# Kernel tuning notes

Hardware: AMD Instinct MI355X
Metric: run time of the kernel (lower is better)

Reference implementation:

```python
import jax, jax.numpy as jnp
import numpy as np
import math

D = 128      # out_dim (= d)
H = 4        # n_heads
DK = D // H  # d_k = 32
M = 5        # fixed num types in forward
NN = 15      # fixed N in forward
SQRT_DK = math.sqrt(DK)


def setup_inputs() -> dict:
    key = jax.random.key(0)
    ks = jax.random.split(key, 18)
    b, n = 1024, 64
    inp = {
        "node_inp": jax.random.normal(ks[0], (D, b, n), jnp.float32),
        "WW": jax.random.normal(ks[1], (b, M, n, NN), jnp.float32) * 0.1,
        "mask_matrix": jax.random.uniform(ks[2], (M * NN, n), jnp.float32),
        "R": jax.random.normal(ks[3], (b, H, n, n), jnp.float32),
        "attn_mask": jax.random.uniform(ks[4], (1, 1, n, 4 * n), jnp.float32),
        # learned parameters (xavier-ish scale)
        "WK": jax.random.normal(ks[5], (M, D, D), jnp.float32) * 0.05,
        "bK": jax.random.normal(ks[6], (M, D, 1), jnp.float32) * 0.05,
        "WQ": jax.random.normal(ks[7], (M, D, D), jnp.float32) * 0.05,
        "bQ": jax.random.normal(ks[8], (M, D, 1), jnp.float32) * 0.05,
        "WM": jax.random.normal(ks[9], (M, D, D), jnp.float32) * 0.05,
        "bM": jax.random.normal(ks[10], (M, D, 1), jnp.float32) * 0.05,
        "WB": jax.random.normal(ks[11], (M, D, D), jnp.float32) * 0.05,
        "bB": jax.random.normal(ks[12], (M, D, 1), jnp.float32) * 0.05,
        "Wmsgup": jax.random.normal(ks[13], (DK, DK), jnp.float32) * 0.1,
        "Wmsgdown": jax.random.normal(ks[14], (DK, DK), jnp.float32) * 0.1,
        "Wmsgleft": jax.random.normal(ks[15], (DK, DK), jnp.float32) * 0.1,
        "Wmsgright": jax.random.normal(ks[16], (DK, DK), jnp.float32) * 0.1,
    }
    return inp


def reference(node_inp, WW, mask_matrix, R, attn_mask,
              WK, bK, WQ, bQ, WM, bM, WB, bB,
              Wmsgup, Wmsgdown, Wmsgleft, Wmsgright):
    d, b, n = node_inp.shape
    # project node features through per-type mixing: (b, m, d, N)
    node_inp_m = jnp.einsum('dbn,bmnN->bmdN', node_inp, WW)

    def proj_perm(W, bias):
        # per-type linear then permute(0,2,1,3) before flatten (as K/Q do)
        x = jnp.einsum('mde,bmeN->bmdN', W, node_inp_m) + bias[None]  # (b,m,d,N)
        x = x.transpose(0, 2, 1, 3).reshape(b, d, M * NN)
        return x @ mask_matrix  # (b, d, n)

    K = proj_perm(WK, bK).reshape(b, H, DK, n)
    Q = proj_perm(WQ, bQ).reshape(b, H, DK, n)

    # message: NOTE original reshapes (b*m,d,N) -> (b,d,m*N) WITHOUT the permute; replicate faithfully
    msg = jnp.einsum('mde,bmeN->bmdN', WM, node_inp_m) + bM[None]  # (b,m,d,N)
    message = msg.reshape(b, d, M * NN) @ mask_matrix               # (b, d, n)

    A = jnp.einsum('bhki,bhkj->bhij', Q, K) / SQRT_DK               # (b,h,n,n)
    aw = jax.nn.softmax(R + A, axis=3)
    aw = jnp.where(jnp.isnan(aw), jnp.zeros_like(aw), aw)
    aw = jnp.tile(aw, (1, 1, 1, 4)) * attn_mask                     # (b,h,n,4n)

    res_msg = message.reshape(b, H, DK, n)
    Wmsg = jnp.concatenate([Wmsgup, Wmsgdown, Wmsgleft, Wmsgright], axis=1)  # (dk, 4dk)
    res = jnp.einsum('kq,bhkn->bhqn', Wmsg, res_msg)                # (b,h,4dk,n)
    res = res.reshape(b, H, DK, 4 * n)                               # faithful reshape

    B = jnp.einsum('bhnm,bhkm->bhkn', aw, res).reshape(b, d, n)
    B = jax.nn.gelu(B, approximate=False)

    Bm = jnp.einsum('bdn,bmnN->bmdN', B, WW)
    Bm = jnp.einsum('mde,bmeN->bmdN', WB, Bm) + bB[None]
    Bm = Bm.transpose(0, 2, 1, 3).reshape(b, d, M * NN) @ mask_matrix  # (b,d,n)
    out = Bm.transpose(1, 0, 2) + node_inp                             # (d,b,n)
    return (out, aw[0, 0])
```

## Files before the change

kernel.cpp:

```cpp
#include <hip/hip_runtime.h>
#include <math.h>

#define Dd 128
#define Hh 4
#define DKk 32
#define Mm 5
#define NNn 15
#define Bb 1024
#define Nn 64
#define MN 75
#define BN 65536
#define RSQRT_DK 0.17677669529663687f

typedef __attribute__((ext_vector_type(8))) short bf16x8;
typedef __attribute__((ext_vector_type(4))) float f32x4;

__device__ __forceinline__ ushort f2bf(float x) {
    unsigned u = __float_as_uint(x);
    u = (u + 0x7fffu + ((u >> 16) & 1u)) >> 16;
    return (ushort)u;
}
__device__ __forceinline__ float bf2f(ushort h) {
    return __uint_as_float(((unsigned)h) << 16);
}
__device__ __forceinline__ void split2(float x, ushort& hi, ushort& lo) {
    hi = f2bf(x);
    lo = f2bf(x - bf2f(hi));
}
__device__ __forceinline__ f32x4 MFMA(bf16x8 a, bf16x8 b, f32x4 c) {
    return __builtin_amdgcn_mfma_f32_16x16x32_bf16(a, b, c, 0, 0, 0);
}

__global__ void k0_prep(const float* __restrict__ maskm,
                        const float* __restrict__ WK, const float* __restrict__ bK,
                        const float* __restrict__ WQ, const float* __restrict__ bQ,
                        const float* __restrict__ WM, const float* __restrict__ bM,
                        const float* __restrict__ WB, const float* __restrict__ bB,
                        const float* __restrict__ Wu, const float* __restrict__ Wd,
                        const float* __restrict__ Wl, const float* __restrict__ Wr,
                        ushort* __restrict__ WKhi, ushort* __restrict__ WKlo,
                        ushort* __restrict__ WQhi, ushort* __restrict__ WQlo,
                        ushort* __restrict__ WMhi, ushort* __restrict__ WBhi,
                        ushort* __restrict__ maskhi, ushort* __restrict__ masklo,
                        ushort* __restrict__ maskThi, ushort* __restrict__ maskTlo,
                        float* __restrict__ btKT, float* __restrict__ btQT,
                        float* __restrict__ btMT, float* __restrict__ btB,
                        ushort* __restrict__ WcatT)
{
    int tid = blockIdx.x * blockDim.x + threadIdx.x;
    int nthr = gridDim.x * blockDim.x;
    const int NW = Mm * Dd * Dd;
    for (int i = tid; i < NW; i += nthr) {
        split2(WK[i], WKhi[i], WKlo[i]);
        split2(WQ[i], WQhi[i], WQlo[i]);
        WMhi[i] = f2bf(WM[i]);
        WBhi[i] = f2bf(WB[i]);
    }
    for (int i = tid; i < 96 * 64; i += nthr) {
        float v = (i < MN * 64) ? maskm[i] : 0.f;
        split2(v, maskhi[i], masklo[i]);
    }
    for (int i = tid; i < 64 * 96; i += nthr) {
        int col = i / 96, j = i - col * 96;
        float v = (j < MN) ? maskm[j * 64 + col] : 0.f;
        split2(v, maskThi[i], maskTlo[i]);
    }
    for (int i = tid; i < 4096; i += nthr) {
        int q = i >> 5, kk = i & 31;
        const float* Wsel = (q < 32) ? Wu : (q < 64) ? Wd : (q < 96) ? Wl : Wr;
        WcatT[i] = f2bf(Wsel[kk * 32 + (q & 31)]);
    }
    for (int i = tid; i < 8192; i += nthr) {
        int d = i >> 6, col = i & 63;
        float aKv = 0.f, aQv = 0.f, aBv = 0.f;
        for (int m = 0; m < Mm; ++m) {
            float mrs = 0.f;
            for (int N = 0; N < NNn; ++N) mrs += maskm[(m * 15 + N) * 64 + col];
            aKv += bK[m * 128 + d] * mrs;
            aQv += bQ[m * 128 + d] * mrs;
            aBv += bB[m * 128 + d] * mrs;
        }
        btKT[col * 128 + d] = aKv;
        btQT[col * 128 + d] = aQv;
        btB[i] = aBv;
        float aMv = 0.f;
        for (int j = 0; j < MN; ++j) {
            int f = d * 75 + j;
            int m = f / 1920;
            int dloc = (f / 15) & 127;
            aMv += bM[m * 128 + dloc] * maskm[j * 64 + col];
        }
        btMT[col * 128 + d] = aMv;
    }
}

__global__ __launch_bounds__(512, 4) void k1_proj(
    const float* __restrict__ node, const float* __restrict__ WW,
    const ushort* __restrict__ WKhi, const ushort* __restrict__ WKlo,
    const ushort* __restrict__ WQhi, const ushort* __restrict__ WQlo,
    const ushort* __restrict__ WMhi,
    const ushort* __restrict__ maskThi, const ushort* __restrict__ maskTlo,
    const float* __restrict__ btKT, const float* __restrict__ btQT,
    const float* __restrict__ btMT,
    ushort* __restrict__ Khi, ushort* __restrict__ Klo,
    ushort* __restrict__ Qhi, ushort* __restrict__ Qlo,
    ushort* __restrict__ msgTg)
{
    const int b = blockIdx.x;
    const int tid = threadIdx.x;
    const int lane = tid & 63, w = tid >> 6;
    const int l15 = lane & 15, lq = lane >> 4;

    __shared__ ushort nimTh[80 * 136];
    __shared__ ushort nimTl[80 * 136];
    __shared__ ushort planes[4 * 32 * 104];

    ushort* Ykh = planes;
    ushort* Ykl = planes + 32 * 104;
    ushort* Yqh = planes + 2 * 32 * 104;
    ushort* Yql = planes + 3 * 32 * 104;

    for (int t = tid; t < 5 * 136; t += 512) {
        int mm = t / 136, e = t - mm * 136;
        nimTh[(mm * 16 + 15) * 136 + e] = 0;
        nimTl[(mm * 16 + 15) * 136 + e] = 0;
    }
    for (int t = tid; t < 128 * 29; t += 512) {
        int r = t / 29, cc = 75 + (t - r * 29);
        planes[r * 104 + cc] = 0;
    }

    const f32x4 zz = {0.f, 0.f, 0.f, 0.f};

    {
        bf16x8 ah[2], al[2];
        #pragma unroll
        for (int ks = 0; ks < 2; ++ks) {
            const float* np = node + (size_t)(w * 16 + l15) * BN + b * 64 + ks * 32 + lq * 8;
            float tmp[8];
            *(float4*)tmp       = *(const float4*)np;
            *(float4*)(tmp + 4) = *(const float4*)(np + 4);
            #pragma unroll
            for (int j = 0; j < 8; ++j) {
                ushort h_, l_; split2(tmp[j], h_, l_);
                ah[ks][j] = (short)h_; al[ks][j] = (short)l_;
            }
        }
        for (int m = 0; m < Mm; ++m) {
            const float* wp = WW + ((size_t)b * Mm + m) * 960 + (l15 < 15 ? l15 : 0);
            f32x4 chh = zz, chl = zz, clh = zz;
            #pragma unroll
            for (int ks = 0; ks < 2; ++ks) {
                bf16x8 bh, bl;
                #pragma unroll
                for (int t = 0; t < 8; ++t) {
                    int n = ks * 32 + lq * 8 + t;
                    float v = (l15 < 15) ? wp[n * 15] : 0.f;
                    ushort h_, l_; split2(v, h_, l_);
                    bh[t] = (short)h_; bl[t] = (short)l_;
                }
                chh = MFMA(ah[ks], bh, chh);
                chl = MFMA(ah[ks], bl, chl);
                clh = MFMA(al[ks], bh, clh);
            }
            f32x4 c = chh + chl + clh;
            if (l15 < 15) {
                #pragma unroll
                for (int t = 0; t < 4; ++t) {
                    int e = w * 16 + lq * 4 + t;
                    split2(c[t], nimTh[(m * 16 + l15) * 136 + e],
                                 nimTl[(m * 16 + l15) * 136 + e]);
                }
            }
        }
    }
    __syncthreads();

    for (int qd = 0; qd < 4; ++qd) {
        for (int u = w; u < 10; u += 8) {
            int m = u >> 1, rt = u & 1;
            int d0 = qd * 32 + rt * 16 + l15;
            f32x4 khh = zz, khl = zz, klh = zz;
            f32x4 qhh = zz, qhl = zz, qlh = zz;
            #pragma unroll
            for (int ks = 0; ks < 4; ++ks) {
                int k0 = ks * 32 + lq * 8;
                size_t wo = (size_t)m * 16384 + (size_t)d0 * 128 + k0;
                bf16x8 akh = *(const bf16x8*)(WKhi + wo);
                bf16x8 akl = *(const bf16x8*)(WKlo + wo);
                bf16x8 aqh = *(const bf16x8*)(WQhi + wo);
                bf16x8 aql = *(const bf16x8*)(WQlo + wo);
                bf16x8 bh = *(const bf16x8*)(&nimTh[(m * 16 + l15) * 136 + k0]);
                bf16x8 bl = *(const bf16x8*)(&nimTl[(m * 16 + l15) * 136 + k0]);
                khh = MFMA(akh, bh, khh); khl = MFMA(akh, bl, khl); klh = MFMA(akl, bh, klh);
                qhh = MFMA(aqh, bh, qhh); qhl = MFMA(aqh, bl, qhl); qlh = MFMA(aql, bh, qlh);
            }
            f32x4 cK = khh + khl + klh;
            f32x4 cQ = qhh + qhl + qlh;
            if (l15 < 15) {
                int j = m * 15 + l15;
                #pragma unroll
                for (int t = 0; t < 4; ++t) {
                    int r = rt * 16 + lq * 4 + t;
                    split2(cK[t], Ykh[r * 104 + j], Ykl[r * 104 + j]);
                    split2(cQ[t], Yqh[r * 104 + j], Yql[r * 104 + j]);
                }
            }
        }
        __syncthreads();
        {
            int nr = w & 3, dc = w >> 2;
            f32x4 khh = zz, khl = zz, klh = zz;
            f32x4 qhh = zz, qhl = zz, qlh = zz;
            #pragma unroll
            for (int ks = 0; ks < 3; ++ks) {
                int k0 = ks * 32 + lq * 8;
                bf16x8 mh = *(const bf16x8*)(maskThi + (nr * 16 + l15) * 96 + k0);
                bf16x8 ml = *(const bf16x8*)(maskTlo + (nr * 16 + l15) * 96 + k0);
                bf16x8 ykh = *(const bf16x8*)(&Ykh[(dc * 16 + l15) * 104 + k0]);
                bf16x8 ykl = *(const bf16x8*)(&Ykl[(dc * 16 + l15) * 104 + k0]);
                bf16x8 yqh = *(const bf16x8*)(&Yqh[(dc * 16 + l15) * 104 + k0]);
                bf16x8 yql = *(const bf16x8*)(&Yql[(dc * 16 + l15) * 104 + k0]);
                khh = MFMA(mh, ykh, khh); khl = MFMA(ml, ykh, khl); klh = MFMA(mh, ykl, klh);
                qhh = MFMA(mh, yqh, qhh); qhl = MFMA(ml, yqh, qhl); qlh = MFMA(mh, yql, qlh);
            }
            f32x4 cK = khh + khl + klh;
            f32x4 cQ = qhh + qhl + qlh;
            #pragma unroll
            for (int t = 0; t < 4; ++t) {
                int n = nr * 16 + lq * 4 + t;
                int dloc = dc * 16 + l15;
                int d = qd * 32 + dloc;
                size_t oi = (((size_t)(b * 4 + qd)) * 64 + n) * 32 + dloc;
                ushort hh_, ll_;
                split2(cK[t] + btKT[n * 128 + d], hh_, ll_);
                Khi[oi] = hh_; Klo[oi] = ll_;
                split2(cQ[t] + btQT[n * 128 + d], hh_, ll_);
                Qhi[oi] = hh_; Qlo[oi] = ll_;
            }
        }
        __syncthreads();
    }

    {
        int rt = w;
        for (int m = 0; m < Mm; ++m) {
            f32x4 c0 = zz, c1 = zz;
            #pragma unroll
            for (int ks = 0; ks < 4; ++ks) {
                int k0 = ks * 32 + lq * 8;
                bf16x8 a  = *(const bf16x8*)(WMhi + (size_t)m * 16384 + (size_t)(rt * 16 + l15) * 128 + k0);
                bf16x8 bh = *(const bf16x8*)(&nimTh[(m * 16 + l15) * 136 + k0]);
                if (ks < 2) c0 = MFMA(a, bh, c0); else c1 = MFMA(a, bh, c1);
            }
            f32x4 c = c0 + c1;
            if (l15 < 15) {
                #pragma unroll
                for (int t = 0; t < 4; ++t) {
                    int dflat = rt * 16 + lq * 4 + t;
                    int g = m * 1920 + dflat * 15 + l15;
                    planes[(g / 75) * 104 + (g % 75)] = f2bf(c[t]);
                }
            }
        }
    }
    __syncthreads();
    #pragma unroll
    for (int s = 0; s < 4; ++s) {
        int u = w * 4 + s;
        int nr = u & 3, ddc = u >> 2;
        f32x4 cs0 = zz, cs1 = zz, cs2 = zz;
        {
            bf16x8 a0 = *(const bf16x8*)(maskThi + (nr * 16 + l15) * 96 + lq * 8);
            bf16x8 b0 = *(const bf16x8*)(&planes[(ddc * 16 + l15) * 104 + lq * 8]);
            cs0 = MFMA(a0, b0, cs0);
            bf16x8 a1 = *(const bf16x8*)(maskThi + (nr * 16 + l15) * 96 + 32 + lq * 8);
            bf16x8 b1 = *(const bf16x8*)(&planes[(ddc * 16 + l15) * 104 + 32 + lq * 8]);
            cs1 = MFMA(a1, b1, cs1);
            bf16x8 a2 = *(const bf16x8*)(maskThi + (nr * 16 + l15) * 96 + 64 + lq * 8);
            bf16x8 b2 = *(const bf16x8*)(&planes[(ddc * 16 + l15) * 104 + 64 + lq * 8]);
            cs2 = MFMA(a2, b2, cs2);
        }
        f32x4 c = cs0 + cs1 + cs2;
        #pragma unroll
        for (int t = 0; t < 4; ++t) {
            int n = nr * 16 + lq * 4 + t;
            int dd = ddc * 16 + l15;
            int h = dd >> 5, dk = dd & 31;
            msgTg[(((size_t)(b * 4 + h)) * 64 + n) * 32 + dk] = f2bf(c[t] + btMT[n * 128 + dd]);
        }
    }
}

__global__ __launch_bounds__(512, 4) void k2_attn(
    const ushort* __restrict__ Khi, const ushort* __restrict__ Klo,
    const ushort* Qhi, const ushort* __restrict__ Qlo,
    const ushort* __restrict__ msgTg,
    const float* __restrict__ R, const float* __restrict__ am,
    const ushort* __restrict__ WcatT, float* __restrict__ aw00,
    ushort* Bout)
{
    const int b = blockIdx.x >> 2, h = blockIdx.x & 3;
    const int tid = threadIdx.x;
    const int lane = tid & 63, w = tid >> 6;
    const int l15 = lane & 15, lq = lane >> 4;

    __shared__ float  ST[64 * 65];
    __shared__ ushort resS[128 * 72];
    __shared__ ushort awq[64 * 72];

    const f32x4 zz = {0.f, 0.f, 0.f, 0.f};
    const size_t base2 = (size_t)(b * 4 + h) * 2048;
    const float* Rb = R + (size_t)(b * 4 + h) * 4096;

    {
        int ti = w >> 1;
        bf16x8 ah = *(const bf16x8*)(Qhi + base2 + (size_t)(ti * 16 + l15) * 32 + lq * 8);
        bf16x8 al = *(const bf16x8*)(Qlo + base2 + (size_t)(ti * 16 + l15) * 32 + lq * 8);
        #pragma unroll
        for (int s = 0; s < 2; ++s) {
            int tj = (w & 1) * 2 + s;
            bf16x8 bh = *(const bf16x8*)(Khi + base2 + (size_t)(tj * 16 + l15) * 32 + lq * 8);
            bf16x8 bl = *(const bf16x8*)(Klo + base2 + (size_t)(tj * 16 + l15) * 32 + lq * 8);
            f32x4 chh = zz, chl = zz, clh = zz;
            chh = MFMA(ah, bh, chh); chl = MFMA(ah, bl, chl); clh = MFMA(al, bh, clh);
            f32x4 c = chh + chl + clh;
            #pragma unroll
            for (int r = 0; r < 4; ++r) {
                int i = ti * 16 + lq * 4 + r, j = tj * 16 + l15;
                ST[j * 65 + i] = Rb[i * 64 + j] + c[r] * RSQRT_DK;
            }
        }
    }
    {
        bf16x8 a = *(const bf16x8*)(WcatT + (w * 16 + l15) * 32 + lq * 8);
        #pragma unroll
        for (int nt = 0; nt < 4; ++nt) {
            bf16x8 bfr = *(const bf16x8*)(msgTg + base2 + (size_t)(nt * 16 + l15) * 32 + lq * 8);
            f32x4 c = MFMA(a, bfr, zz);
            #pragma unroll
            for (int r = 0; r < 4; ++r)
                resS[(w * 16 + lq * 4 + r) * 72 + nt * 16 + l15] = f2bf(c[r]);
        }
    }
    __syncthreads();

    {
        int row = tid >> 3, part = tid & 7;
        float v[8]; float mx = -INFINITY;
        #pragma unroll
        for (int jj = 0; jj < 8; ++jj) { v[jj] = ST[(part * 8 + jj) * 65 + row]; mx = fmaxf(mx, v[jj]); }
        mx = fmaxf(mx, __shfl_xor(mx, 1));
        mx = fmaxf(mx, __shfl_xor(mx, 2));
        mx = fmaxf(mx, __shfl_xor(mx, 4));
        float s = 0.f;
        #pragma unroll
        for (int jj = 0; jj < 8; ++jj) { v[jj] = expf(v[jj] - mx); s += v[jj]; }
        s += __shfl_xor(s, 1); s += __shfl_xor(s, 2); s += __shfl_xor(s, 4);
        float inv = 1.f / s;
        #pragma unroll
        for (int jj = 0; jj < 8; ++jj) {
            float p = v[jj] * inv;
            ST[(part * 8 + jj) * 65 + row] = isnan(p) ? 0.f : p;
        }
    }
    __syncthreads();

    const int kt = w >> 2, it = w & 3;
    f32x4 accB0 = zz, accB1 = zz;
    for (int q = 0; q < 4; ++q) {
        for (int e = tid; e < 4096; e += 512) {
            int i = e >> 6, j0 = e & 63;
            float p = ST[j0 * 65 + i] * am[i * 256 + q * 64 + j0];
            awq[i * 72 + j0] = f2bf(p);
            if (blockIdx.x == 0) aw00[i * 256 + q * 64 + j0] = p;
        }
        __syncthreads();
        int row = 4 * (kt * 16 + l15) + q;
        bf16x8 a0 = *(const bf16x8*)(&resS[row * 72 + lq * 8]);
        bf16x8 b0 = *(const bf16x8*)(&awq[(it * 16 + l15) * 72 + lq * 8]);
        accB0 = MFMA(a0, b0, accB0);
        bf16x8 a1 = *(const bf16x8*)(&resS[row * 72 + 32 + lq * 8]);
        bf16x8 b1 = *(const bf16x8*)(&awq[(it * 16 + l15) * 72 + 32 + lq * 8]);
        accB1 = MFMA(a1, b1, accB1);
        __syncthreads();
    }
    f32x4 accB = accB0 + accB1;

    #pragma unroll
    for (int r = 0; r < 4; ++r) {
        int k = kt * 16 + lq * 4 + r, i = it * 16 + l15;
        float x = accB[r];
        float g = 0.5f * x * (1.f + erff(x * 0.70710678118654752f));
        Bout[base2 + k * 64 + i] = f2bf(g);
    }
}

__global__ __launch_bounds__(512, 4) void k3_out(
    const ushort* Bbuf, const float* __restrict__ WW,
    const ushort* __restrict__ WBhi, const ushort* __restrict__ maskhi,
    const float* __restrict__ btB, const float* __restrict__ node,
    float* __restrict__ outp)
{
    const int b = blockIdx.x, tid = threadIdx.x;
    const int lane = tid & 63, w = tid >> 6, l15 = lane & 15, lq = lane >> 4;
    __shared__ ushort sB[128 * 72];
    __shared__ ushort wwh[64 * 17];
    __shared__ ushort t1[128 * 17];
    __shared__ ushort nm[32 * 66];

    for (int i = tid; i < 8192; i += 512) {
        int d = i >> 6, n = i & 63;
        sB[d * 72 + n] = Bbuf[(size_t)b * 8192 + i];
    }
    const f32x4 zz = {0.f, 0.f, 0.f, 0.f};
    f32x4 acc[4];
    for (int c = 0; c < 4; ++c) acc[c] = zz;
    __syncthreads();

    for (int m = 0; m < Mm; ++m) {
        for (int i = tid; i < 64 * 17; i += 512) {
            int n = i / 17, N = i - n * 17;
            wwh[i] = (N < 15) ? f2bf(WW[(((size_t)b * Mm + m) * 64 + n) * 15 + N]) : (ushort)0;
        }
        __syncthreads();
        {
            f32x4 c0 = zz, c1 = zz;
            #pragma unroll
            for (int ks = 0; ks < 2; ++ks) {
                int k0 = ks * 32 + (lq << 3);
                bf16x8 a = *(const bf16x8*)(&sB[(w * 16 + l15) * 72 + k0]);
                bf16x8 bh;
                #pragma unroll
                for (int t = 0; t < 8; ++t) bh[t] = (short)wwh[(k0 + t) * 17 + l15];
                if (ks == 0) c0 = MFMA(a, bh, c0); else c1 = MFMA(a, bh, c1);
            }
            f32x4 c = c0 + c1;
            #pragma unroll
            for (int t = 0; t < 4; ++t)
                t1[(w * 16 + lq * 4 + t) * 17 + l15] = f2bf(c[t]);
        }
        __syncthreads();

        bf16x8 mfh;
        {
            int ct = w & 3;
            int k0 = lq << 3;
            #pragma unroll
            for (int t = 0; t < 8; ++t) {
                int kk = k0 + t;
                int row = (kk < 15) ? (m * 15 + kk) : 95;
                mfh[t] = (short)maskhi[row * 64 + ct * 16 + l15];
            }
        }
        for (int eb = 0; eb < 4; ++eb) {
            {
                int rtl = w >> 2, ct = w & 3;
                int e = eb * 32 + rtl * 16 + l15;
                int k0 = lq << 3;
                bf16x8 a;
                #pragma unroll
                for (int t = 0; t < 8; ++t) {
                    int kk = k0 + t;
                    int cc = (kk < 15) ? kk : 15;
                    a[t] = (short)t1[e * 17 + cc];
                }
                f32x4 c = zz;
                c = MFMA(a, mfh, c);
                #pragma unroll
                for (int t = 0; t < 4; ++t)
                    nm[(rtl * 16 + lq * 4 + t) * 66 + ct * 16 + l15] = f2bf(c[t]);
            }
            __syncthreads();
            {
                size_t aoff = (size_t)(w * 16 + l15) * 128 + eb * 32 + (lq << 3);
                bf16x8 a = *(const bf16x8*)(WBhi + m * 16384 + aoff);
                int k0 = lq << 3;
                #pragma unroll
                for (int ct = 0; ct < 4; ++ct) {
                    bf16x8 bh;
                    #pragma unroll
                    for (int t = 0; t < 8; ++t) bh[t] = (short)nm[(k0 + t) * 66 + ct * 16 + l15];
                    acc[ct] = MFMA(a, bh, acc[ct]);
                }
            }
            __syncthreads();
        }
    }
    #pragma unroll
    for (int ct = 0; ct < 4; ++ct) {
        #pragma unroll
        for (int t = 0; t < 4; ++t) {
            int d = w * 16 + lq * 4 + t;
            int col = ct * 16 + l15;
            size_t gi = (size_t)d * BN + b * 64 + col;
            outp[gi] = acc[ct][t] + btB[d * 64 + col] + node[gi];
        }
    }
}

extern "C" void kernel_launch(void* const* d_in, const int* in_sizes, int n_in,
                              void* d_out, int out_size, void* d_ws, size_t ws_size,
                              hipStream_t stream) {
    const float* node  = (const float*)d_in[0];
    const float* WW    = (const float*)d_in[1];
    const float* maskm = (const float*)d_in[2];
    const float* R     = (const float*)d_in[3];
    const float* am    = (const float*)d_in[4];
    const float* WK = (const float*)d_in[5];  const float* bK = (const float*)d_in[6];
    const float* WQ = (const float*)d_in[7];  const float* bQ = (const float*)d_in[8];
    const float* WM = (const float*)d_in[9];  const float* bM = (const float*)d_in[10];
    const float* WB = (const float*)d_in[11]; const float* bB = (const float*)d_in[12];
    const float* Wu = (const float*)d_in[13]; const float* Wd = (const float*)d_in[14];
    const float* Wl = (const float*)d_in[15]; const float* Wr = (const float*)d_in[16];

    float* out  = (float*)d_out;
    float* aw00 = out + (size_t)Dd * BN;

    ushort* Khi = (ushort*)d_out;
    ushort* Klo = Khi + 8388608;

    char* W = (char*)d_ws;
    ushort* Qhi   = (ushort*)W;
    ushort* Qlo   = Qhi + 8388608;
    ushort* msgTg = Qlo + 8388608;
    ushort* WKhi  = msgTg + 8388608;
    ushort* WKlo  = WKhi + 81920;
    ushort* WQhi  = WKlo + 81920;
    ushort* WQlo  = WQhi + 81920;
    ushort* WMhi  = WQlo + 81920;
    ushort* WBhi  = WMhi + 81920;
    ushort* maskhi  = WBhi + 81920;
    ushort* masklo  = maskhi + 6144;
    ushort* maskThi = masklo + 6144;
    ushort* maskTlo = maskThi + 6144;
    ushort* WcatT   = maskTlo + 6144;
    float*  btKT = (float*)(WcatT + 4096);
    float*  btQT = btKT + 8192;
    float*  btMT = btQT + 8192;
    float*  btB  = btMT + 8192;

    k0_prep<<<512, 256, 0, stream>>>(maskm, WK, bK, WQ, bQ, WM, bM, WB, bB,
                                     Wu, Wd, Wl, Wr,
                                     WKhi, WKlo, WQhi, WQlo, WMhi, WBhi,
                                     maskhi, masklo, maskThi, maskTlo,
                                     btKT, btQT, btMT, btB, WcatT);
    k1_proj<<<Bb, 512, 0, stream>>>(node, WW, WKhi, WKlo, WQhi, WQlo, WMhi,
                                    maskThi, maskTlo, btKT, btQT, btMT,
                                    Khi, Klo, Qhi, Qlo, msgTg);
    k2_attn<<<Bb * Hh, 512, 0, stream>>>(Khi, Klo, Qhi, Qlo, msgTg, R, am,
                                         WcatT, aw00, Qhi );
    k3_out<<<Bb, 512, 0, stream>>>(Qhi , WW, WBhi, maskhi, btB, node, out);
}
```

Measured before the change: 279.7 us.

## Cut barriers and LDS traffic across projection, attention and output kernels

In k1, the WW tile is staged into shared memory with coalesced float4 loads, the node tile uses an XOR-swizzled layout instead of padding, and K and Q work is split between two warp groups so each wave keeps fewer accumulators. In k2, the per-quarter awq staging buffer and its barriers are dropped: each lane builds its attention-weight B operand directly from the score tile and the mask, and the aw00 output is written in a separate pass. In k3, all WW slices are staged once up front and the mask-multiply stage is done for all of e at once, replacing the per-eb barrier loop. Occupancy hints are raised on k2 and k3. These changes shrink shared-memory footprints and barrier counts, at the cost of some register pressure and extra shared-memory use in k3.

```diff
diff --git a/kernel.cpp b/kernel.cpp
--- a/kernel.cpp
+++ b/kernel.cpp
@@ -30,6 +30,8 @@
 __device__ __forceinline__ f32x4 MFMA(bf16x8 a, bf16x8 b, f32x4 c) {
     return __builtin_amdgcn_mfma_f32_16x16x32_bf16(a, b, c, 0, 0, 0);
 }
+
+#define NSWZ(r, c) ((r) * 128 + ((c) ^ (((r) & 7) << 3)))
 
 __global__ void k0_prep(const float* __restrict__ maskm,
                         const float* __restrict__ WK, const float* __restrict__ bK,
@@ -111,26 +113,29 @@
     const int lane = tid & 63, w = tid >> 6;
     const int l15 = lane & 15, lq = lane >> 4;
 
-    __shared__ ushort nimTh[80 * 136];
-    __shared__ ushort nimTl[80 * 136];
-    __shared__ ushort planes[4 * 32 * 104];
+    __shared__ ushort nimTh[80 * 128];
+    __shared__ ushort nimTl[80 * 128];
+    __shared__ ushort planes[4 * 32 * 96];
 
     ushort* Ykh = planes;
-    ushort* Ykl = planes + 32 * 104;
-    ushort* Yqh = planes + 2 * 32 * 104;
-    ushort* Yql = planes + 3 * 32 * 104;
-
-    for (int t = tid; t < 5 * 136; t += 512) {
-        int mm = t / 136, e = t - mm * 136;
-        nimTh[(mm * 16 + 15) * 136 + e] = 0;
-        nimTl[(mm * 16 + 15) * 136 + e] = 0;
-    }
-    for (int t = tid; t < 128 * 29; t += 512) {
-        int r = t / 29, cc = 75 + (t - r * 29);
-        planes[r * 104 + cc] = 0;
-    }
+    ushort* Ykl = planes + 32 * 96;
+    ushort* Yqh = planes + 2 * 32 * 96;
+    ushort* Yql = planes + 3 * 32 * 96;
+    float* wwRaw = (float*)planes;
 
     const f32x4 zz = {0.f, 0.f, 0.f, 0.f};
+
+    {
+        const float4* src = (const float4*)(WW + (size_t)b * 4800);
+        float4* dst = (float4*)wwRaw;
+        for (int i = tid; i < 1200; i += 512) dst[i] = src[i];
+        for (int t = tid; t < 5 * 128; t += 512) {
+            int mm = t >> 7, e = t & 127;
+            nimTh[(mm * 16 + 15) * 128 + e] = 0;
+            nimTl[(mm * 16 + 15) * 128 + e] = 0;
+        }
+    }
+    __syncthreads();
 
     {
         bf16x8 ah[2], al[2];
@@ -147,7 +152,6 @@
             }
         }
         for (int m = 0; m < Mm; ++m) {
-            const float* wp = WW + ((size_t)b * Mm + m) * 960 + (l15 < 15 ? l15 : 0);
             f32x4 chh = zz, chl = zz, clh = zz;
             #pragma unroll
             for (int ks = 0; ks < 2; ++ks) {
@@ -155,7 +159,7 @@
                 #pragma unroll
                 for (int t = 0; t < 8; ++t) {
                     int n = ks * 32 + lq * 8 + t;
-                    float v = (l15 < 15) ? wp[n * 15] : 0.f;
+                    float v = (l15 < 15) ? wwRaw[m * 960 + n * 15 + l15] : 0.f;
                     ushort h_, l_; split2(v, h_, l_);
                     bh[t] = (short)h_; bl[t] = (short)l_;
                 }
@@ -168,64 +172,71 @@
                 #pragma unroll
                 for (int t = 0; t < 4; ++t) {
                     int e = w * 16 + lq * 4 + t;
-                    split2(c[t], nimTh[(m * 16 + l15) * 136 + e],
-                                 nimTl[(m * 16 + l15) * 136 + e]);
+                    int row = m * 16 + l15;
+                    split2(c[t], nimTh[NSWZ(row, e)], nimTl[NSWZ(row, e)]);
                 }
             }
         }
     }
     __syncthreads();
 
+    const int grp = w >> 2, wl = w & 3;
+    const ushort* Whi = grp ? WQhi : WKhi;
+    const ushort* Wlo = grp ? WQlo : WKlo;
+    const float*  btP = grp ? btQT : btKT;
+    ushort* Phi = grp ? Qhi : Khi;
+    ushort* Plo = grp ? Qlo : Klo;
+    ushort* Yh = grp ? Yqh : Ykh;
+    ushort* Yl = grp ? Yql : Ykl;
+
     for (int qd = 0; qd < 4; ++qd) {
-        for (int u = w; u < 10; u += 8) {
+        if (qd == 0) {
+            for (int t = tid; t < 128 * 21; t += 512) {
+                int r = t / 21, cc = 75 + (t - r * 21);
+                planes[r * 96 + cc] = 0;
+            }
+        }
+        for (int u = wl; u < 10; u += 4) {
             int m = u >> 1, rt = u & 1;
             int d0 = qd * 32 + rt * 16 + l15;
-            f32x4 khh = zz, khl = zz, klh = zz;
-            f32x4 qhh = zz, qhl = zz, qlh = zz;
+            f32x4 phh = zz, phl = zz, plh = zz;
             #pragma unroll
             for (int ks = 0; ks < 4; ++ks) {
                 int k0 = ks * 32 + lq * 8;
                 size_t wo = (size_t)m * 16384 + (size_t)d0 * 128 + k0;
-                bf16x8 akh = *(const bf16x8*)(WKhi + wo);
-                bf16x8 akl = *(const bf16x8*)(WKlo + wo);
-                bf16x8 aqh = *(const bf16x8*)(WQhi + wo);
-                bf16x8 aql = *(const bf16x8*)(WQlo + wo);
-                bf16x8 bh = *(const bf16x8*)(&nimTh[(m * 16 + l15) * 136 + k0]);
-                bf16x8 bl = *(const bf16x8*)(&nimTl[(m * 16 + l15) * 136 + k0]);
-                khh = MFMA(akh, bh, khh); khl = MFMA(akh, bl, khl); klh = MFMA(akl, bh, klh);
-                qhh = MFMA(aqh, bh, qhh); qhl = MFMA(aqh, bl, qhl); qlh = MFMA(aql, bh, qlh);
-            }
-            f32x4 cK = khh + khl + klh;
-            f32x4 cQ = qhh + qhl + qlh;
+                bf16x8 awh = *(const bf16x8*)(Whi + wo);
+                bf16x8 awl = *(const bf16x8*)(Wlo + wo);
+                int nrow = m * 16 + l15;
+                bf16x8 bh = *(const bf16x8*)(&nimTh[NSWZ(nrow, k0)]);
+                bf16x8 bl = *(const bf16x8*)(&nimTl[NSWZ(nrow, k0)]);
+                phh = MFMA(awh, bh, phh); phl = MFMA(awh, bl, phl); plh = MFMA(awl, bh, plh);
+            }
+            f32x4 c = phh + phl + plh;
             if (l15 < 15) {
                 int j = m * 15 + l15;
                 #pragma unroll
                 for (int t = 0; t < 4; ++t) {
                     int r = rt * 16 + lq * 4 + t;
-                    split2(cK[t], Ykh[r * 104 + j], Ykl[r * 104 + j]);
-                    split2(cQ[t], Yqh[r * 104 + j], Yql[r * 104 + j]);
+                    split2(c[t], Yh[r * 96 + j], Yl[r * 96 + j]);
                 }
             }
         }
         __syncthreads();
-        {
-            int nr = w & 3, dc = w >> 2;
-            f32x4 khh = zz, khl = zz, klh = zz;
-            f32x4 qhh = zz, qhl = zz, qlh = zz;
+        #pragma unroll
+        for (int s = 0; s < 2; ++s) {
+            int u = wl * 2 + s;
+            int nr = u & 3, dc = u >> 2;
+            f32x4 phh = zz, phl = zz, plh = zz;
             #pragma unroll
             for (int ks = 0; ks < 3; ++ks) {
                 int k0 = ks * 32 + lq * 8;
                 bf16x8 mh = *(const bf16x8*)(maskThi + (nr * 16 + l15) * 96 + k0);
                 bf16x8 ml = *(const bf16x8*)(maskTlo + (nr * 16 + l15) * 96 + k0);
-                bf16x8 ykh = *(const bf16x8*)(&Ykh[(dc * 16 + l15) * 104 + k0]);
-                bf16x8 ykl = *(const bf16x8*)(&Ykl[(dc * 16 + l15) * 104 + k0]);
-                bf16x8 yqh = *(const bf16x8*)(&Yqh[(dc * 16 + l15) * 104 + k0]);
-                bf16x8 yql = *(const bf16x8*)(&Yql[(dc * 16 + l15) * 104 + k0]);
-                khh = MFMA(mh, ykh, khh); khl = MFMA(ml, ykh, khl); klh = MFMA(mh, ykl, klh);
-                qhh = MFMA(mh, yqh, qhh); qhl = MFMA(ml, yqh, qhl); qlh = MFMA(mh, yql, qlh);
-            }
-            f32x4 cK = khh + khl + klh;
-            f32x4 cQ = qhh + qhl + qlh;
+                bf16x8 yh = *(const bf16x8*)(&Yh[(dc * 16 + l15) * 96 + k0]);
+                bf16x8 yl = *(const bf16x8*)(&Yl[(dc * 16 + l15) * 96 + k0]);
+                phh = MFMA(mh, yh, phh); phl = MFMA(ml, yh, phl); plh = MFMA(mh, yl, plh);
+            }
+            f32x4 c = phh + phl + plh;
             #pragma unroll
             for (int t = 0; t < 4; ++t) {
                 int n = nr * 16 + lq * 4 + t;
@@ -233,10 +244,8 @@
                 int d = qd * 32 + dloc;
                 size_t oi = (((size_t)(b * 4 + qd)) * 64 + n) * 32 + dloc;
                 ushort hh_, ll_;
-                split2(cK[t] + btKT[n * 128 + d], hh_, ll_);
-                Khi[oi] = hh_; Klo[oi] = ll_;
-                split2(cQ[t] + btQT[n * 128 + d], hh_, ll_);
-                Qhi[oi] = hh_; Qlo[oi] = ll_;
+                split2(c[t] + btP[n * 128 + d], hh_, ll_);
+                Phi[oi] = hh_; Plo[oi] = ll_;
             }
         }
         __syncthreads();
@@ -250,7 +259,8 @@
             for (int ks = 0; ks < 4; ++ks) {
                 int k0 = ks * 32 + lq * 8;
                 bf16x8 a  = *(const bf16x8*)(WMhi + (size_t)m * 16384 + (size_t)(rt * 16 + l15) * 128 + k0);
-                bf16x8 bh = *(const bf16x8*)(&nimTh[(m * 16 + l15) * 136 + k0]);
+                int nrow = m * 16 + l15;
+                bf16x8 bh = *(const bf16x8*)(&nimTh[NSWZ(nrow, k0)]);
                 if (ks < 2) c0 = MFMA(a, bh, c0); else c1 = MFMA(a, bh, c1);
             }
             f32x4 c = c0 + c1;
@@ -259,7 +269,7 @@
                 for (int t = 0; t < 4; ++t) {
                     int dflat = rt * 16 + lq * 4 + t;
                     int g = m * 1920 + dflat * 15 + l15;
-                    planes[(g / 75) * 104 + (g % 75)] = f2bf(c[t]);
+                    planes[(g / 75) * 96 + (g % 75)] = f2bf(c[t]);
                 }
             }
         }
@@ -272,13 +282,13 @@
         f32x4 cs0 = zz, cs1 = zz, cs2 = zz;
         {
             bf16x8 a0 = *(const bf16x8*)(maskThi + (nr * 16 + l15) * 96 + lq * 8);
-            bf16x8 b0 = *(const bf16x8*)(&planes[(ddc * 16 + l15) * 104 + lq * 8]);
+            bf16x8 b0 = *(const bf16x8*)(&planes[(ddc * 16 + l15) * 96 + lq * 8]);
             cs0 = MFMA(a0, b0, cs0);
             bf16x8 a1 = *(const bf16x8*)(maskThi + (nr * 16 + l15) * 96 + 32 + lq * 8);
-            bf16x8 b1 = *(const bf16x8*)(&planes[(ddc * 16 + l15) * 104 + 32 + lq * 8]);
+            bf16x8 b1 = *(const bf16x8*)(&planes[(ddc * 16 + l15) * 96 + 32 + lq * 8]);
             cs1 = MFMA(a1, b1, cs1);
             bf16x8 a2 = *(const bf16x8*)(maskThi + (nr * 16 + l15) * 96 + 64 + lq * 8);
-            bf16x8 b2 = *(const bf16x8*)(&planes[(ddc * 16 + l15) * 104 + 64 + lq * 8]);
+            bf16x8 b2 = *(const bf16x8*)(&planes[(ddc * 16 + l15) * 96 + 64 + lq * 8]);
             cs2 = MFMA(a2, b2, cs2);
         }
         f32x4 c = cs0 + cs1 + cs2;
@@ -292,7 +302,7 @@
     }
 }
 
-__global__ __launch_bounds__(512, 4) void k2_attn(
+__global__ __launch_bounds__(512, 8) void k2_attn(
     const ushort* __restrict__ Khi, const ushort* __restrict__ Klo,
     const ushort* Qhi, const ushort* __restrict__ Qlo,
     const ushort* __restrict__ msgTg,
@@ -307,7 +317,6 @@
 
     __shared__ float  ST[64 * 65];
     __shared__ ushort resS[128 * 72];
-    __shared__ ushort awq[64 * 72];
 
     const f32x4 zz = {0.f, 0.f, 0.f, 0.f};
     const size_t base2 = (size_t)(b * 4 + h) * 2048;
@@ -366,37 +375,51 @@
     }
     __syncthreads();
 
+    if (blockIdx.x == 0) {
+        for (int t = tid; t < 16384; t += 512) {
+            int i = t >> 8, j = t & 255;
+            aw00[t] = ST[(j & 63) * 65 + i] * am[t];
+        }
+    }
+
     const int kt = w >> 2, it = w & 3;
+    const int i_col = it * 16 + l15;
     f32x4 accB0 = zz, accB1 = zz;
     for (int q = 0; q < 4; ++q) {
-        for (int e = tid; e < 4096; e += 512) {
-            int i = e >> 6, j0 = e & 63;
-            float p = ST[j0 * 65 + i] * am[i * 256 + q * 64 + j0];
-            awq[i * 72 + j0] = f2bf(p);
-            if (blockIdx.x == 0) aw00[i * 256 + q * 64 + j0] = p;
-        }
-        __syncthreads();
         int row = 4 * (kt * 16 + l15) + q;
         bf16x8 a0 = *(const bf16x8*)(&resS[row * 72 + lq * 8]);
-        bf16x8 b0 = *(const bf16x8*)(&awq[(it * 16 + l15) * 72 + lq * 8]);
+        bf16x8 a1 = *(const bf16x8*)(&resS[row * 72 + 32 + lq * 8]);
+        float amv[8];
+        bf16x8 b0, b1;
+        *(float4*)amv       = *(const float4*)(am + i_col * 256 + q * 64 + lq * 8);
+        *(float4*)(amv + 4) = *(const float4*)(am + i_col * 256 + q * 64 + lq * 8 + 4);
+        #pragma unroll
+        for (int jj = 0; jj < 8; ++jj) {
+            int j0 = lq * 8 + jj;
+            b0[jj] = (short)f2bf(ST[j0 * 65 + i_col] * amv[jj]);
+        }
+        *(float4*)amv       = *(const float4*)(am + i_col * 256 + q * 64 + 32 + lq * 8);
+        *(float4*)(amv + 4) = *(const float4*)(am + i_col * 256 + q * 64 + 32 + lq * 8 + 4);
+        #pragma unroll
+        for (int jj = 0; jj < 8; ++jj) {
+            int j0 = 32 + lq * 8 + jj;
+            b1[jj] = (short)f2bf(ST[j0 * 65 + i_col] * amv[jj]);
+        }
         accB0 = MFMA(a0, b0, accB0);
-        bf16x8 a1 = *(const bf16x8*)(&resS[row * 72 + 32 + lq * 8]);
-        bf16x8 b1 = *(const bf16x8*)(&awq[(it * 16 + l15) * 72 + 32 + lq * 8]);
         accB1 = MFMA(a1, b1, accB1);
-        __syncthreads();
     }
     f32x4 accB = accB0 + accB1;
 
     #pragma unroll
     for (int r = 0; r < 4; ++r) {
-        int k = kt * 16 + lq * 4 + r, i = it * 16 + l15;
+        int k = kt * 16 + lq * 4 + r;
         float x = accB[r];
         float g = 0.5f * x * (1.f + erff(x * 0.70710678118654752f));
-        Bout[base2 + k * 64 + i] = f2bf(g);
-    }
-}
-
-__global__ __launch_bounds__(512, 4) void k3_out(
+        Bout[base2 + k * 64 + i_col] = f2bf(g);
+    }
+}
+
+__global__ __launch_bounds__(512, 6) void k3_out(
     const ushort* Bbuf, const float* __restrict__ WW,
     const ushort* __restrict__ WBhi, const ushort* __restrict__ maskhi,
     const float* __restrict__ btB, const float* __restrict__ node,
@@ -405,13 +428,22 @@
     const int b = blockIdx.x, tid = threadIdx.x;
     const int lane = tid & 63, w = tid >> 6, l15 = lane & 15, lq = lane >> 4;
     __shared__ ushort sB[128 * 72];
-    __shared__ ushort wwh[64 * 17];
+    __shared__ ushort wwAll[5 * 16 * 72];
     __shared__ ushort t1[128 * 17];
-    __shared__ ushort nm[32 * 66];
+    __shared__ ushort nm[128 * 72];
 
     for (int i = tid; i < 8192; i += 512) {
         int d = i >> 6, n = i & 63;
         sB[d * 72 + n] = Bbuf[(size_t)b * 8192 + i];
+    }
+    for (int i = tid; i < 4800; i += 512) {
+        int m = i / 960, r = i - m * 960;
+        int n = r / 15, N = r - n * 15;
+        wwAll[(m * 16 + N) * 72 + n] = f2bf(WW[(size_t)b * 4800 + i]);
+    }
+    for (int i = tid; i < 5 * 72; i += 512) {
+        int m = i / 72, n = i - m * 72;
+        wwAll[(m * 16 + 15) * 72 + n] = 0;
     }
     const f32x4 zz = {0.f, 0.f, 0.f, 0.f};
     f32x4 acc[4];
@@ -419,60 +451,46 @@
     __syncthreads();
 
     for (int m = 0; m < Mm; ++m) {
-        for (int i = tid; i < 64 * 17; i += 512) {
-            int n = i / 17, N = i - n * 17;
-            wwh[i] = (N < 15) ? f2bf(WW[(((size_t)b * Mm + m) * 64 + n) * 15 + N]) : (ushort)0;
+        {
+            f32x4 c0 = zz, c1 = zz;
+            #pragma unroll
+            for (int ks = 0; ks < 2; ++ks) {
+                int k0 = ks * 32 + (lq << 3);
+                bf16x8 a  = *(const bf16x8*)(&sB[(w * 16 + l15) * 72 + k0]);
+                bf16x8 bh = *(const bf16x8*)(&wwAll[(m * 16 + l15) * 72 + k0]);
+                if (ks == 0) c0 = MFMA(a, bh, c0); else c1 = MFMA(a, bh, c1);
+            }
+            f32x4 c = c0 + c1;
+            #pragma unroll
+            for (int t = 0; t < 4; ++t)
+                t1[(w * 16 + lq * 4 + t) * 17 + l15] = f2bf(c[t]);
         }
         __syncthreads();
         {
-            f32x4 c0 = zz, c1 = zz;
-            #pragma unroll
-            for (int ks = 0; ks < 2; ++ks) {
-                int k0 = ks * 32 + (lq << 3);
-                bf16x8 a = *(const bf16x8*)(&sB[(w * 16 + l15) * 72 + k0]);
-                bf16x8 bh;
-                #pragma unroll
-                for (int t = 0; t < 8; ++t) bh[t] = (short)wwh[(k0 + t) * 17 + l15];
-                if (ks == 0) c0 = MFMA(a, bh, c0); else c1 = MFMA(a, bh, c1);
-            }
-            f32x4 c = c0 + c1;
-            #pragma unroll
-            for (int t = 0; t < 4; ++t)
-                t1[(w * 16 + lq * 4 + t) * 17 + l15] = f2bf(c[t]);
-        }
-        __syncthreads();
-
-        bf16x8 mfh;
-        {
-            int ct = w & 3;
-            int k0 = lq << 3;
-            #pragma unroll
-            for (int t = 0; t < 8; ++t) {
-                int kk = k0 + t;
-                int row = (kk < 15) ? (m * 15 + kk) : 95;
-                mfh[t] = (short)maskhi[row * 64 + ct * 16 + l15];
-            }
-        }
-        for (int eb = 0; eb < 4; ++eb) {
-            {
-                int rtl = w >> 2, ct = w & 3;
-                int e = eb * 32 + rtl * 16 + l15;
+            #pragma unroll
+            for (int s = 0; s < 4; ++s) {
+                int u = w * 4 + s;
+                int et = u & 7, ct = u >> 3;
                 int k0 = lq << 3;
-                bf16x8 a;
+                bf16x8 a, mfh;
                 #pragma unroll
                 for (int t = 0; t < 8; ++t) {
                     int kk = k0 + t;
                     int cc = (kk < 15) ? kk : 15;
-                    a[t] = (short)t1[e * 17 + cc];
+                    a[t] = (short)t1[(et * 16 + l15) * 17 + cc];
+                    int row = (kk < 15) ? (m * 15 + kk) : 95;
+                    mfh[t] = (short)maskhi[row * 64 + ct * 16 + l15];
                 }
-                f32x4 c = zz;
-                c = MFMA(a, mfh, c);
+                f32x4 c = MFMA(a, mfh, zz);
                 #pragma unroll
                 for (int t = 0; t < 4; ++t)
-                    nm[(rtl * 16 + lq * 4 + t) * 66 + ct * 16 + l15] = f2bf(c[t]);
-            }
-            __syncthreads();
-            {
+                    nm[(et * 16 + lq * 4 + t) * 72 + ct * 16 + l15] = f2bf(c[t]);
+            }
+        }
+        __syncthreads();
+        {
+            #pragma unroll
+            for (int eb = 0; eb < 4; ++eb) {
                 size_t aoff = (size_t)(w * 16 + l15) * 128 + eb * 32 + (lq << 3);
                 bf16x8 a = *(const bf16x8*)(WBhi + m * 16384 + aoff);
                 int k0 = lq << 3;
@@ -480,12 +498,13 @@
                 for (int ct = 0; ct < 4; ++ct) {
                     bf16x8 bh;
                     #pragma unroll
-                    for (int t = 0; t < 8; ++t) bh[t] = (short)nm[(k0 + t) * 66 + ct * 16 + l15];
+                    for (int t = 0; t < 8; ++t)
+                        bh[t] = (short)nm[(eb * 32 + k0 + t) * 72 + ct * 16 + l15];
                     acc[ct] = MFMA(a, bh, acc[ct]);
                 }
             }
-            __syncthreads();
-        }
+        }
+        __syncthreads();
     }
     #pragma unroll
     for (int ct = 0; ct < 4; ++ct) {
```

Measured after the change: 324.1 us. +15.9%, slower.
